# Kernel optimization log

Hardware: AMD Instinct MI355X
Metric: run time of the kernel (lower is better)

The kernel has to match this reference:

```python
import jax, jax.numpy as jnp
import numpy as np

IN_F, OUT_F, K = 64, 64, 3
EPS = 1e-05
C_EQ = 1.0 / np.sqrt(IN_F * K * K)  # equalized-lr constant


def setup_inputs() -> dict:
    key = jax.random.key(0)
    k1, k2 = jax.random.split(key)
    x = jax.random.normal(k1, (16, IN_F, 256, 256), dtype=jnp.float32)
    weight = jax.random.normal(k2, (OUT_F, IN_F, K, K), dtype=jnp.float32)
    return {"x": x, "weight": weight}


def reference(x, weight):
    # Equalized-lr scaling
    w = weight * jnp.asarray(C_EQ, dtype=weight.dtype)  # [O, I, K, K]
    # Demodulation: per-output-channel rsqrt of sum of squares over (I, K, K).
    # With no style modulation the factor is identical for every sample, so the
    # original groups=batch conv is exactly a plain conv2d with these weights.
    sigma_inv = jax.lax.rsqrt(jnp.sum(w * w, axis=(1, 2, 3), keepdims=True) + EPS)
    w = w * sigma_inv  # [O, I, K, K]
    out = jax.lax.conv_general_dilated(
        x, w,
        window_strides=(1, 1),
        padding=[(1, 1), (1, 1)],  # (k-1)//2 = 1
        dimension_numbers=("NCHW", "OIHW", "NCHW"),
    )
    return out  # [B, O, H, W]
```

## Files before the change

kernel.cpp:

```cpp
#include <hip/hip_runtime.h>
#include <hip/hip_bf16.h>
#include <math.h>

#define BATCH 16
#define ICH 64
#define OCH 64
#define HH 256
#define WW 256
#define HW 65536
#define EPS 1e-5f
#define C_EQ (1.0f / 24.0f)

typedef __attribute__((ext_vector_type(8))) short short8;
typedef __attribute__((ext_vector_type(4))) float floatx4;

#define AFRAG_BYTES 73728
#define XT_PIX 258
#define XT_ROWB (XT_PIX * 128)
#define XT_IMGB ((size_t)XT_PIX * XT_PIX * 128)
#define WS_NEEDED (AFRAG_BYTES + (size_t)BATCH * XT_IMGB)

#define AS1 __attribute__((address_space(1)))
#define AS3 __attribute__((address_space(3)))

static __device__ __forceinline__ unsigned short f2bf(float v) {
    __hip_bfloat16 b = __float2bfloat16(v);
    return *reinterpret_cast<unsigned short*>(&b);
}
static __device__ __forceinline__ unsigned int pk2(float a, float b) {
    return (unsigned int)f2bf(a) | ((unsigned int)f2bf(b) << 16);
}

__global__ void weight_prep_kernel(const float* __restrict__ wgt,
                                   unsigned int* __restrict__ wsout)
{
    const int tid = threadIdx.x;
    const int oc  = blockIdx.x * 16 + (tid >> 2);
    const int q   = tid & 3;
    const float* wb = wgt + ((size_t)oc * 64 + q * 16) * 9;

    float s = 0.f;
    #pragma unroll 4
    for (int i = 0; i < 36; ++i) {
        const float4 v = reinterpret_cast<const float4*>(wb)[i];
        s += v.x*v.x + v.y*v.y + v.z*v.z + v.w*v.w;
    }
    s += __shfl_xor(s, 1, 64);
    s += __shfl_xor(s, 2, 64);
    const float sc = C_EQ * rsqrtf(s * (C_EQ * C_EQ) + EPS);

    const int h = q >> 1;
    #pragma unroll
    for (int s2 = 0; s2 < 2; ++s2) {
        const int G = (q & 1) * 2 + s2;
        #pragma unroll
        for (int jp = 0; jp < 4; ++jp) {
            const float* r0 = wb + (8 * s2 + 2 * jp) * 9;
            const float* r1 = r0 + 9;
            #pragma unroll
            for (int t = 0; t < 9; ++t) {
                const unsigned int d = (unsigned)f2bf(r0[t] * sc)
                                     | ((unsigned)f2bf(r1[t] * sc) << 16);
                wsout[(((h * 9 + t) * 64 + oc) * 4 + G) * 4 + jp] = d;
            }
        }
    }
}

__global__ __launch_bounds__(256, 8) void transpose_pad_kernel(
    const float* __restrict__ x, char* __restrict__ xT)
{
    const int tid  = threadIdx.x;
    const int lane = tid & 63;
    const int wvv  = tid >> 6;
    const int cb = blockIdx.x, hh = blockIdx.y, b = blockIdx.z;
    char* rowbase = xT + (size_t)b * XT_IMGB + (size_t)hh * XT_ROWB;
    const uint4 z4 = make_uint4(0u, 0u, 0u, 0u);

    if (hh == 0 || hh == XT_PIX - 1) {
        char* base = rowbase + (size_t)(cb * 64 + 1) * 128;
        *reinterpret_cast<uint4*>(base + tid * 32)      = z4;
        *reinterpret_cast<uint4*>(base + tid * 32 + 16) = z4;
        if (cb == 0 && tid < 8)
            *reinterpret_cast<uint4*>(rowbase + tid * 16) = z4;
        if (cb == 3 && tid >= 8 && tid < 16)
            *reinterpret_cast<uint4*>(rowbase + (size_t)257 * 128 + (tid - 8) * 16) = z4;
        return;
    }
    if (cb == 0 && tid < 8)
        *reinterpret_cast<uint4*>(rowbase + tid * 16) = z4;
    if (cb == 3 && tid >= 8 && tid < 16)
        *reinterpret_cast<uint4*>(rowbase + (size_t)257 * 128 + (tid - 8) * 16) = z4;

    __shared__ float lds[64 * 65];
    const int h = hh - 1;
    const float* xrow = x + (size_t)b * ICH * HW + (size_t)h * WW + cb * 64;
    float v[16];
    #pragma unroll
    for (int i = 0; i < 16; ++i)
        v[i] = xrow[(size_t)(i * 4 + wvv) * HW + lane];
    #pragma unroll
    for (int i = 0; i < 16; ++i)
        lds[lane * 65 + i * 4 + wvv] = v[i];
    __syncthreads();

    const int col = tid >> 2;
    const int g   = tid & 3;
    const float* lp = &lds[col * 65];
    char* dst = rowbase + (size_t)(cb * 64 + col + 1) * 128;
    #pragma unroll
    for (int r = 0; r < 2; ++r) {
        const int ich = r * 32 + g * 8;
        uint4 dw;
        dw.x = pk2(lp[ich + 0], lp[ich + 1]);
        dw.y = pk2(lp[ich + 2], lp[ich + 3]);
        dw.z = pk2(lp[ich + 4], lp[ich + 5]);
        dw.w = pk2(lp[ich + 6], lp[ich + 7]);
        *reinterpret_cast<uint4*>(dst + r * 64 + g * 16) = dw;
    }
}

__global__ __launch_bounds__(256, 3) void conv_mfma_ogsplit(
    const char* __restrict__ ws, float* __restrict__ out)
{
    __shared__ __align__(16) char lx[6 * 8448];

    const int tid  = threadIdx.x;
    const int lane = tid & 63;
    const int wv   = tid >> 6;
    const int n_l  = lane & 15;
    const int G_l  = lane >> 4;

    const int bid = blockIdx.x;
    const int wg  = (bid & 7) * 512 + (bid >> 3);
    const int b   = wg >> 8;
    const int cbk = (wg >> 6) & 3;
    const int ry  = wg & 63;
    const int gc0 = cbk * 64;
    const int gr0 = ry * 4;

    const char* xTb = ws + AFRAG_BYTES + (size_t)b * XT_IMGB;
    const unsigned abase = (unsigned)((wv << 10) + (n_l << 6) + (G_l << 4));

    const unsigned laneoff = ((unsigned)(lane >> 3) << 7)
                           + ((unsigned)((lane & 7) ^ (lane >> 3)) << 4);
    #pragma unroll
    for (int t = 0; t < 14; ++t) {
        const int i = wv + 4 * t;
        if (i >= 54) break;
        const int row = i / 9;
        const int k   = i - row * 9;
        const char* src = xTb + (size_t)(gr0 + row) * XT_ROWB
                        + ((unsigned)gc0 << 7) + ((unsigned)k << 10) + laneoff;
        if (k < 8 || lane < 16)
            __builtin_amdgcn_global_load_lds(
                (const AS1 void*)src,
                (AS3 void*)&lx[row * 8448 + (k << 10)], 16, 0, 0);
    }

    short8 A[9];
#define LOADA(idx, kc) A[idx] = *reinterpret_cast<const short8*>(ws + ((kc) << 12) + abase)
    #pragma unroll
    for (int kc = 0; kc < 9; ++kc) LOADA(kc, kc);

    floatx4 acc[4][4];
    #pragma unroll
    for (int cb = 0; cb < 4; ++cb)
        #pragma unroll
        for (int fr = 0; fr < 4; ++fr) acc[cb][fr] = (floatx4){0.f, 0.f, 0.f, 0.f};

    __syncthreads();

    #pragma unroll
    for (int ph = 0; ph < 6; ++ph) {
        const int kw = ph % 3, h = ph / 3;
        if (ph >= 1 && ph <= 3) {
            const int r = ph - 1;
            LOADA(r,     9 + r);
            LOADA(r + 3, 12 + r);
            LOADA(r + 6, 15 + r);
        }
        #pragma unroll
        for (int cb = 0; cb < 4; ++cb) {
            const int px = cb * 16 + n_l + kw;
            const int bo = (px << 7) + ((((h << 2) | G_l) ^ (px & 7)) << 4);
            uint4 B[6];
            #pragma unroll
            for (int j = 0; j < 6; ++j)
                B[j] = *reinterpret_cast<const uint4*>(&lx[j * 8448 + bo]);
            #pragma unroll
            for (int kh = 0; kh < 3; ++kh) {
                const short8 a = A[kh * 3 + kw];
                #pragma unroll
                for (int fr = 0; fr < 4; ++fr)
                    acc[cb][fr] = __builtin_amdgcn_mfma_f32_16x16x32_bf16(
                        a, __builtin_bit_cast(short8, B[fr + kh]), acc[cb][fr], 0, 0, 0);
            }
        }
    }
#undef LOADA

    float* lf = (float*)lx;
    #pragma unroll
    for (int half = 0; half < 2; ++half) {
        __syncthreads();
        if ((wv >> 1) == half) {
            const int ocl16 = (wv & 1) << 4;
            #pragma unroll
            for (int cb = 0; cb < 4; ++cb)
                #pragma unroll
                for (int fr = 0; fr < 4; ++fr)
                    #pragma unroll
                    for (int ri = 0; ri < 4; ++ri)
                        lf[((ocl16 + (G_l << 2) + ri) * 4 + fr) * 68 + cb * 16 + n_l]
                            = acc[cb][fr][ri];
        }
        __syncthreads();
        const int q = tid & 15;
        #pragma unroll
        for (int j = 0; j < 8; ++j) {
            const int row = (tid >> 4) + (j << 4);
            const int ocl = row >> 2, fr = row & 3;
            const float4 v = *reinterpret_cast<const float4*>(&lf[row * 68 + (q << 2)]);
            float* op = out + ((size_t)b * OCH + half * 32 + ocl) * HW
                            + (size_t)(gr0 + fr) * WW + gc0 + (q << 2);
            *reinterpret_cast<float4*>(op) = v;
        }
    }
}

#define TR 4
#define TC 64
#define XROWS 6
#define XCOLS 66
#define XPIXB 64
#define XROWB (XCOLS * XPIXB)
#define XHALFB (XROWS * XROWB)
#define LDS_BYTES (2 * XHALFB)

__global__ __launch_bounds__(256, 2) void conv_mfma_fallback(
    const float* __restrict__ x,
    const unsigned int* __restrict__ wfrag,
    float* __restrict__ out)
{
    __shared__ __align__(16) char lds[LDS_BYTES];
    const int tid  = threadIdx.x;
    const int lane = tid & 63;
    const int wv   = tid >> 6;
    const int n_l  = lane & 15;
    const int G_l  = lane >> 4;

    short8 afrag[18];
    {
        const int oc_l = (wv << 4) + n_l;
        const char* wsb = (const char*)wfrag;
        #pragma unroll
        for (int kc = 0; kc < 18; ++kc)
            afrag[kc] = *reinterpret_cast<const short8*>(
                wsb + (((kc * 64 + oc_l) * 4 + G_l) << 4));
    }

    const int gr0 = blockIdx.y * TR;
    const int gc0 = blockIdx.x * TC;
    const int b   = blockIdx.z;
    const float* xb = x + (size_t)b * ICH * HW;

    for (int p = wv; p < 48; p += 4) {
        const int h  = p / 24;
        const int pr = (p % 24) >> 2;
        const int G  = p & 3;
        const int gr = gr0 - 1 + pr;
        const int icb = h * 32 + G * 8;
        const bool rok = ((unsigned)gr < (unsigned)HH);
        {
            const float* src = xb + (size_t)icb * HW + (size_t)gr * WW + gc0 + lane;
            float v[8];
            #pragma unroll
            for (int qq = 0; qq < 8; ++qq) v[qq] = rok ? src[(size_t)qq * HW] : 0.f;
            const int pc = lane + 1;
            const int addr = h*XHALFB + pr*XROWB + pc*XPIXB + ((G ^ ((pc >> 1) & 3)) << 4);
            uint4 w4; w4.x = pk2(v[0], v[1]); w4.y = pk2(v[2], v[3]);
            w4.z = pk2(v[4], v[5]); w4.w = pk2(v[6], v[7]);
            *reinterpret_cast<uint4*>(&lds[addr]) = w4;
        }
        if (lane < 2) {
            const int pc = lane * 65;
            const int gc = gc0 - 1 + pc;
            const bool ok = rok && ((unsigned)gc < (unsigned)WW);
            const float* src = xb + (size_t)icb * HW + (size_t)gr * WW + gc;
            float v[8];
            #pragma unroll
            for (int qq = 0; qq < 8; ++qq) v[qq] = ok ? src[(size_t)qq * HW] : 0.f;
            const int addr = h*XHALFB + pr*XROWB + pc*XPIXB + ((G ^ ((pc >> 1) & 3)) << 4);
            uint4 w4; w4.x = pk2(v[0], v[1]); w4.y = pk2(v[2], v[3]);
            w4.z = pk2(v[4], v[5]); w4.w = pk2(v[6], v[7]);
            *reinterpret_cast<uint4*>(&lds[addr]) = w4;
        }
    }
    __syncthreads();

    int colp[4][3];
    #pragma unroll
    for (int cbq = 0; cbq < 4; ++cbq)
        #pragma unroll
        for (int kw = 0; kw < 3; ++kw) {
            const int pcv = cbq * 16 + n_l + kw;
            colp[cbq][kw] = pcv * XPIXB + ((G_l ^ ((pcv >> 1) & 3)) << 4);
        }

    floatx4 acc[16];
    #pragma unroll
    for (int f = 0; f < 16; ++f) acc[f] = (floatx4){0.f, 0.f, 0.f, 0.f};

    #pragma unroll
    for (int kc = 0; kc < 18; ++kc) {
        const int h = kc / 9, tap = kc % 9;
        const int kh = tap / 3, kw = tap % 3;
        #pragma unroll
        for (int f = 0; f < 16; ++f) {
            const int fr = f >> 2, cbq = f & 3;
            const short8 bfrag = *reinterpret_cast<const short8*>(
                &lds[h*XHALFB + (fr + kh)*XROWB + colp[cbq][kw]]);
            acc[f] = __builtin_amdgcn_mfma_f32_16x16x32_bf16(afrag[kc], bfrag, acc[f], 0, 0, 0);
        }
    }

    float* ob = out + ((size_t)(b*OCH + (wv << 4) + (G_l << 2)) * HW)
                    + (size_t)gr0 * WW + gc0 + n_l;
    #pragma unroll
    for (int f = 0; f < 16; ++f) {
        const int fr = f >> 2, cbq = f & 3;
        #pragma unroll
        for (int ri = 0; ri < 4; ++ri)
            ob[(size_t)ri * HW + fr * WW + cbq * 16] = acc[f][ri];
    }
}

extern "C" void kernel_launch(void* const* d_in, const int* in_sizes, int n_in,
                              void* d_out, int out_size, void* d_ws, size_t ws_size,
                              hipStream_t stream) {
    const float* x = (const float*)d_in[0];
    const float* w = (const float*)d_in[1];
    float* out = (float*)d_out;
    unsigned int* wsf = (unsigned int*)d_ws;

    weight_prep_kernel<<<dim3(4), 64, 0, stream>>>(w, wsf);

    if (ws_size >= WS_NEEDED) {
        char* xT = (char*)d_ws + AFRAG_BYTES;
        transpose_pad_kernel<<<dim3(4, XT_PIX, BATCH), 256, 0, stream>>>(x, xT);
        conv_mfma_ogsplit<<<dim3(4096), 256, 0, stream>>>((const char*)d_ws, out);
    } else {
        conv_mfma_fallback<<<dim3(4, 64, BATCH), 256, 0, stream>>>(x, wsf, out);
    }
}
```

Before: 207.4 us.

## Switch conv main loop to 32x32x16 bf16 MFMA with new weight fragment layout

Replaces the 16x16x32 MFMA tiling in the implicit-GEMM conv with 32x32x16 MFMA. Each wave now covers 32 output channels by 32 pixels, and the weight-prep kernel writes a second weight-fragment layout to match. The larger instruction is meant to cut the number of LDS B-fragment reads and instructions per FLOP. In exchange the K loop has 12 phases instead of 6, and the epilogue register-to-LDS mapping is rewritten, which risks register pressure and LDS bank conflicts.

```diff
diff --git a/kernel.cpp b/kernel.cpp
--- a/kernel.cpp
+++ b/kernel.cpp
@@ -13,12 +13,15 @@
 
 typedef __attribute__((ext_vector_type(8))) short short8;
 typedef __attribute__((ext_vector_type(4))) float floatx4;
+typedef __attribute__((ext_vector_type(16))) float floatx16;
 
 #define AFRAG_BYTES 73728
+#define A2_OFF 73728
+#define XT_OFF 147456
 #define XT_PIX 258
 #define XT_ROWB (XT_PIX * 128)
 #define XT_IMGB ((size_t)XT_PIX * XT_PIX * 128)
-#define WS_NEEDED (AFRAG_BYTES + (size_t)BATCH * XT_IMGB)
+#define WS_NEEDED ((size_t)XT_OFF + (size_t)BATCH * XT_IMGB)
 
 #define AS1 __attribute__((address_space(1)))
 #define AS3 __attribute__((address_space(3)))
@@ -63,6 +66,18 @@
                                      | ((unsigned)f2bf(r1[t] * sc) << 16);
                 wsout[(((h * 9 + t) * 64 + oc) * 4 + G) * 4 + jp] = d;
             }
+        }
+    }
+    unsigned int* w2 = wsout + (A2_OFF / 4);
+    #pragma unroll
+    for (int g = 0; g < 2; ++g) {
+        #pragma unroll
+        for (int t = 0; t < 9; ++t) {
+            const int idx16 = ((q * 9 + t) * 2 + (oc >> 5)) * 64 + ((oc & 31) + (g << 5));
+            #pragma unroll
+            for (int jp = 0; jp < 4; ++jp)
+                w2[idx16 * 4 + jp] = pk2(wb[(8*g + 2*jp) * 9 + t] * sc,
+                                         wb[(8*g + 2*jp + 1) * 9 + t] * sc);
         }
     }
 }
@@ -120,7 +135,7 @@
     }
 }
 
-__global__ __launch_bounds__(256, 3) void conv_mfma_ogsplit(
+__global__ __launch_bounds__(256, 3) void conv_mfma_32(
     const char* __restrict__ ws, float* __restrict__ out)
 {
     __shared__ __align__(16) char lx[6 * 8448];
@@ -128,8 +143,9 @@
     const int tid  = threadIdx.x;
     const int lane = tid & 63;
     const int wv   = tid >> 6;
-    const int n_l  = lane & 15;
-    const int G_l  = lane >> 4;
+    const int och  = wv & 1;
+    const int ch   = wv >> 1;
+    const int gl   = lane >> 5;
 
     const int bid = blockIdx.x;
     const int wg  = (bid & 7) * 512 + (bid >> 3);
@@ -139,8 +155,7 @@
     const int gc0 = cbk * 64;
     const int gr0 = ry * 4;
 
-    const char* xTb = ws + AFRAG_BYTES + (size_t)b * XT_IMGB;
-    const unsigned abase = (unsigned)((wv << 10) + (n_l << 6) + (G_l << 4));
+    const char* xTb = ws + XT_OFF + (size_t)b * XT_IMGB;
 
     const unsigned laneoff = ((unsigned)(lane >> 3) << 7)
                            + ((unsigned)((lane & 7) ^ (lane >> 3)) << 4);
@@ -158,72 +173,78 @@
                 (AS3 void*)&lx[row * 8448 + (k << 10)], 16, 0, 0);
     }
 
+    const unsigned abase2 = (unsigned)((och << 10) + (lane << 4));
     short8 A[9];
-#define LOADA(idx, kc) A[idx] = *reinterpret_cast<const short8*>(ws + ((kc) << 12) + abase)
-    #pragma unroll
-    for (int kc = 0; kc < 9; ++kc) LOADA(kc, kc);
-
-    floatx4 acc[4][4];
-    #pragma unroll
-    for (int cb = 0; cb < 4; ++cb)
-        #pragma unroll
-        for (int fr = 0; fr < 4; ++fr) acc[cb][fr] = (floatx4){0.f, 0.f, 0.f, 0.f};
+#define LOADA2(j, q) A[j] = *reinterpret_cast<const short8*>( \
+    ws + A2_OFF + (((q) * 9 + (j)) << 11) + abase2)
+    #pragma unroll
+    for (int j = 0; j < 9; ++j) LOADA2(j, 0);
+
+    int pxb[3], px7[3];
+    #pragma unroll
+    for (int kw = 0; kw < 3; ++kw) {
+        const int px = (ch << 5) + (lane & 31) + kw;
+        pxb[kw] = px << 7;
+        px7[kw] = px & 7;
+    }
+
+    floatx16 acc[4];
+    #pragma unroll
+    for (int fr = 0; fr < 4; ++fr)
+        #pragma unroll
+        for (int r = 0; r < 16; ++r) acc[fr][r] = 0.f;
 
     __syncthreads();
 
     #pragma unroll
-    for (int ph = 0; ph < 6; ++ph) {
-        const int kw = ph % 3, h = ph / 3;
-        if (ph >= 1 && ph <= 3) {
-            const int r = ph - 1;
-            LOADA(r,     9 + r);
-            LOADA(r + 3, 12 + r);
-            LOADA(r + 6, 15 + r);
-        }
-        #pragma unroll
-        for (int cb = 0; cb < 4; ++cb) {
-            const int px = cb * 16 + n_l + kw;
-            const int bo = (px << 7) + ((((h << 2) | G_l) ^ (px & 7)) << 4);
-            uint4 B[6];
-            #pragma unroll
-            for (int j = 0; j < 6; ++j)
-                B[j] = *reinterpret_cast<const uint4*>(&lx[j * 8448 + bo]);
-            #pragma unroll
-            for (int kh = 0; kh < 3; ++kh) {
-                const short8 a = A[kh * 3 + kw];
-                #pragma unroll
-                for (int fr = 0; fr < 4; ++fr)
-                    acc[cb][fr] = __builtin_amdgcn_mfma_f32_16x16x32_bf16(
-                        a, __builtin_bit_cast(short8, B[fr + kh]), acc[cb][fr], 0, 0, 0);
-            }
-        }
-    }
-#undef LOADA
+    for (int p = 0; p < 12; ++p) {
+        const int q = p / 3, kw = p % 3;
+        if (p >= 1 && p <= 9) {
+            const int kwp = (p - 1) % 3, qp = (p - 1) / 3 + 1;
+            LOADA2(kwp,     qp);
+            LOADA2(kwp + 3, qp);
+            LOADA2(kwp + 6, qp);
+        }
+        uint4 B[6];
+        const int so = ((q << 1) | gl);
+        #pragma unroll
+        for (int j = 0; j < 6; ++j)
+            B[j] = *reinterpret_cast<const uint4*>(
+                &lx[j * 8448 + pxb[kw] + ((so ^ px7[kw]) << 4)]);
+        #pragma unroll
+        for (int kh = 0; kh < 3; ++kh) {
+            const short8 a = A[kh * 3 + kw];
+            #pragma unroll
+            for (int fr = 0; fr < 4; ++fr)
+                acc[fr] = __builtin_amdgcn_mfma_f32_32x32x16_bf16(
+                    a, __builtin_bit_cast(short8, B[fr + kh]), acc[fr], 0, 0, 0);
+        }
+    }
+#undef LOADA2
 
     float* lf = (float*)lx;
     #pragma unroll
     for (int half = 0; half < 2; ++half) {
         __syncthreads();
-        if ((wv >> 1) == half) {
-            const int ocl16 = (wv & 1) << 4;
-            #pragma unroll
-            for (int cb = 0; cb < 4; ++cb)
+        if (och == half) {
+            const int col = (ch << 5) + (lane & 31);
+            #pragma unroll
+            for (int fr = 0; fr < 4; ++fr)
                 #pragma unroll
-                for (int fr = 0; fr < 4; ++fr)
-                    #pragma unroll
-                    for (int ri = 0; ri < 4; ++ri)
-                        lf[((ocl16 + (G_l << 2) + ri) * 4 + fr) * 68 + cb * 16 + n_l]
-                            = acc[cb][fr][ri];
+                for (int r = 0; r < 16; ++r) {
+                    const int ocl = (r & 3) + ((r >> 2) << 3) + (gl << 2);
+                    lf[(ocl * 4 + fr) * 68 + col] = acc[fr][r];
+                }
         }
         __syncthreads();
-        const int q = tid & 15;
+        const int qq = tid & 15;
         #pragma unroll
         for (int j = 0; j < 8; ++j) {
             const int row = (tid >> 4) + (j << 4);
             const int ocl = row >> 2, fr = row & 3;
-            const float4 v = *reinterpret_cast<const float4*>(&lf[row * 68 + (q << 2)]);
+            const float4 v = *reinterpret_cast<const float4*>(&lf[row * 68 + (qq << 2)]);
             float* op = out + ((size_t)b * OCH + half * 32 + ocl) * HW
-                            + (size_t)(gr0 + fr) * WW + gc0 + (q << 2);
+                            + (size_t)(gr0 + fr) * WW + gc0 + (qq << 2);
             *reinterpret_cast<float4*>(op) = v;
         }
     }
@@ -347,9 +368,9 @@
     weight_prep_kernel<<<dim3(4), 64, 0, stream>>>(w, wsf);
 
     if (ws_size >= WS_NEEDED) {
-        char* xT = (char*)d_ws + AFRAG_BYTES;
+        char* xT = (char*)d_ws + XT_OFF;
         transpose_pad_kernel<<<dim3(4, XT_PIX, BATCH), 256, 0, stream>>>(x, xT);
-        conv_mfma_ogsplit<<<dim3(4096), 256, 0, stream>>>((const char*)d_ws, out);
+        conv_mfma_32<<<dim3(4096), 256, 0, stream>>>((const char*)d_ws, out);
     } else {
         conv_mfma_fallback<<<dim3(4, 64, BATCH), 256, 0, stream>>>(x, wsf, out);
     }
```

Measured after the change: 249.2 us. +20.1%, slower.
